# Optimization experiments

Measured on AMD Instinct MI355X. Metric: run time of the kernel, lower is better.

## Reference

```python
import jax, jax.numpy as jnp
import numpy as np

LN_EPS = 1e-5


def setup_inputs() -> dict:
    key = jax.random.key(0)
    k1, k2, k3, k4 = jax.random.split(key, 4)
    B, S, H, NH = 32, 256, 4096, 16
    scale = (2.0 ** 0.5) * ((3.0 / H) ** 0.5)
    inp = jax.random.normal(k1, (B, S, H), dtype=jnp.float32)
    mask = jax.random.randint(k2, (B, S), 0, 2, dtype=jnp.int32)  # 1 = padded key
    weight = jnp.ones((H,), dtype=jnp.float32)
    bias = jnp.zeros((H,), dtype=jnp.float32)
    qkv = jax.random.normal(k3, (H, 3 * H), dtype=jnp.float32) * scale
    o = jax.random.normal(k4, (H, H), dtype=jnp.float32) * scale
    return {"inp": inp, "mask": mask, "weight": weight, "bias": bias,
            "qkv": qkv, "o": o, "isPre": 1}


def _layer_norm(x, weight, bias):
    mu = jnp.mean(x, axis=-1, keepdims=True)
    var = jnp.mean(jnp.square(x - mu), axis=-1, keepdims=True)
    return (x - mu) * jax.lax.rsqrt(var + LN_EPS) * weight + bias


def _mha(x, mask, weight, bias, qkv, o, isPre, head_num=16):
    B, S, H = x.shape
    D = H // head_num
    xn = _layer_norm(x, weight, bias) if isPre else x
    # fused QKV projection: [B,S,3H]
    proj = jnp.einsum('bsh,hk->bsk', xn, qkv)
    q, k, v = jnp.split(proj, 3, axis=-1)
    q = q.reshape(B, S, head_num, D)
    k = k.reshape(B, S, head_num, D)
    v = v.reshape(B, S, head_num, D)
    scores = jnp.einsum('bqnd,bknd->bnqk', q, k) / jnp.sqrt(jnp.float32(D))
    # mask[b,k]==1 -> key k is padding, exclude from softmax
    neg = jnp.finfo(scores.dtype).min
    scores = jnp.where(mask[:, None, None, :] != 0, neg, scores)
    attn = jax.nn.softmax(scores, axis=-1)
    ctx = jnp.einsum('bnqk,bknd->bqnd', attn, v).reshape(B, S, H)
    out = jnp.einsum('bsh,ho->bso', ctx, o)
    if not isPre:
        out = _layer_norm(out, weight, bias)
    return out


def reference(inp, mask, weight, bias, qkv, o, isPre):
    return _mha(inp, mask, weight, bias, qkv, o, bool(isPre))
```

## Files before the change

kernel.cpp:

```cpp
#include <hip/hip_runtime.h>
#include <stdint.h>

typedef unsigned short u16;
typedef short bf16x8 __attribute__((ext_vector_type(8)));
typedef float f32x4 __attribute__((ext_vector_type(4)));
typedef unsigned short u16x8 __attribute__((ext_vector_type(8)));

#define MFMA16(a, b, c) __builtin_amdgcn_mfma_f32_16x16x32_bf16((a), (b), (c), 0, 0, 0)

#define GLOAD_LDS16(gp, lp)                                                        \
  __builtin_amdgcn_global_load_lds((const __attribute__((address_space(1))) void*)(gp), \
                                   (__attribute__((address_space(3))) void*)(lp), 16, 0, 0)

#define BARRIER asm volatile("s_barrier" ::: "memory")
#define WAITV(n) asm volatile("s_waitcnt vmcnt(" #n ")" ::: "memory")
#define WAITL0 asm volatile("s_waitcnt lgkmcnt(0)" ::: "memory")

__device__ __forceinline__ u16 f2bf(float x) {
  union { float f; uint32_t u; } v; v.f = x;
  uint32_t r = (v.u + 0x7FFFu + ((v.u >> 16) & 1u)) >> 16;
  return (u16)r;
}

__device__ __forceinline__ void do_transpose(const float* __restrict__ in,
                                             u16* __restrict__ out, int R, int C,
                                             int bid, float (*tile)[65], int t) {
  int nCt = C >> 6;
  int r0 = (bid / nCt) << 6, c0 = (bid % nCt) << 6;
  int r = t >> 2, cg = (t & 3) << 4;
  const float* src = in + (size_t)(r0 + r) * C + c0 + cg;
#pragma unroll
  for (int i = 0; i < 4; i++) {
    float4 v = *reinterpret_cast<const float4*>(src + (i << 2));
    tile[r][cg + (i << 2) + 0] = v.x; tile[r][cg + (i << 2) + 1] = v.y;
    tile[r][cg + (i << 2) + 2] = v.z; tile[r][cg + (i << 2) + 3] = v.w;
  }
  __syncthreads();
  int c = t >> 2, rg = (t & 3) << 4;
  u16* dst = out + (size_t)(c0 + c) * R + r0 + rg;
#pragma unroll
  for (int i = 0; i < 2; i++) {
    u16x8 o8;
#pragma unroll
    for (int j2 = 0; j2 < 8; j2++) o8[j2] = f2bf(tile[rg + (i << 3) + j2][c]);
    *reinterpret_cast<u16x8*>(dst + (i << 3)) = o8;
  }
}

__device__ __forceinline__ void do_ln(const float* __restrict__ in,
                                      const float* __restrict__ w,
                                      const float* __restrict__ bia,
                                      u16* __restrict__ out, int row,
                                      float* red, int t) {
  const float* x = in + (size_t)row * 4096;
  float4 v[4];
  float s = 0.f, sq = 0.f;
#pragma unroll
  for (int i = 0; i < 4; i++) {
    v[i] = *reinterpret_cast<const float4*>(x + i * 1024 + t * 4);
    s  += v[i].x + v[i].y + v[i].z + v[i].w;
    sq += v[i].x * v[i].x + v[i].y * v[i].y + v[i].z * v[i].z + v[i].w * v[i].w;
  }
#pragma unroll
  for (int off = 32; off > 0; off >>= 1) { s += __shfl_down(s, off); sq += __shfl_down(sq, off); }
  int wid = t >> 6, lane = t & 63;
  if (lane == 0) { red[wid] = s; red[4 + wid] = sq; }
  __syncthreads();
  if (t == 0) {
    float st = red[0] + red[1] + red[2] + red[3];
    float sqt = red[4] + red[5] + red[6] + red[7];
    float mu = st * (1.f / 4096.f);
    float var = sqt * (1.f / 4096.f) - mu * mu;
    red[0] = mu; red[1] = rsqrtf(var + 1e-5f);
  }
  __syncthreads();
  float mu = red[0], rs = red[1];
#pragma unroll
  for (int i = 0; i < 4; i++) {
    float4 wv = *reinterpret_cast<const float4*>(w + i * 1024 + t * 4);
    float4 bv = *reinterpret_cast<const float4*>(bia + i * 1024 + t * 4);
    ushort4 u;
    u.x = f2bf((v[i].x - mu) * rs * wv.x + bv.x);
    u.y = f2bf((v[i].y - mu) * rs * wv.y + bv.y);
    u.z = f2bf((v[i].z - mu) * rs * wv.z + bv.z);
    u.w = f2bf((v[i].w - mu) * rs * wv.w + bv.w);
    *reinterpret_cast<ushort4*>(out + (size_t)row * 4096 + i * 1024 + t * 4) = u;
  }
}

__global__ __launch_bounds__(256) void prep_fused(const float* __restrict__ qkvw, u16* __restrict__ qkvT,
                                                  const float* __restrict__ ow, u16* __restrict__ oT,
                                                  const float* __restrict__ inp, const float* __restrict__ w,
                                                  const float* __restrict__ bia, u16* __restrict__ xn) {
  __shared__ float tile[64][65];
  int bid = blockIdx.x, t = threadIdx.x;
  if (bid < 12288)      do_transpose(qkvw, qkvT, 4096, 12288, bid, tile, t);
  else if (bid < 16384) do_transpose(ow, oT, 4096, 4096, bid - 12288, tile, t);
  else                  do_ln(inp, w, bia, xn, bid - 16384, &tile[0][0], t);
}


#define LDA8(AR, Ab, mh) do {                                                     \
  _Pragma("unroll")                                                               \
  for (int mf = 0; mf < 4; mf++) {                                                \
    int lr = (mh)*128 + wm64 + mf*16 + llo;                                       \
    const char* rb = (Ab) + lr*128;                                               \
    int sw = (lr & 7) << 4;                                                       \
    AR[mf*2+0] = *reinterpret_cast<const bf16x8*>(rb + ((lhi16) ^ sw));           \
    AR[mf*2+1] = *reinterpret_cast<const bf16x8*>(rb + ((64 + lhi16) ^ sw));      \
  }                                                                               \
} while (0)

#define LDB4(BR, Bb, nh) do {                                                     \
  _Pragma("unroll")                                                               \
  for (int nf = 0; nf < 2; nf++) {                                                \
    int lr = (nh)*128 + wn32 + nf*16 + llo;                                       \
    const char* rb = (Bb) + lr*128;                                               \
    int sw = (lr & 7) << 4;                                                       \
    BR[nf*2+0] = *reinterpret_cast<const bf16x8*>(rb + ((lhi16) ^ sw));           \
    BR[nf*2+1] = *reinterpret_cast<const bf16x8*>(rb + ((64 + lhi16) ^ sw));      \
  }                                                                               \
} while (0)

#define MMAQ(AR, BR, mh, nh) do {                                                 \
  _Pragma("unroll")                                                               \
  for (int mf = 0; mf < 4; mf++)                                                  \
    _Pragma("unroll")                                                             \
    for (int nf = 0; nf < 2; nf++) {                                              \
      acc[(mh)*4+mf][(nh)*2+nf] = MFMA16(AR[mf*2+0], BR[nf*2+0], acc[(mh)*4+mf][(nh)*2+nf]); \
      acc[(mh)*4+mf][(nh)*2+nf] = MFMA16(AR[mf*2+1], BR[nf*2+1], acc[(mh)*4+mf][(nh)*2+nf]); \
    }                                                                             \
} while (0)

#define STAGE(isB, h, cbuf, ktile) do {                                           \
  const u16* g_ = (isB) ? Bt : A;                                                 \
  int base0_ = (isB) ? n0 : m0;                                                   \
  char* lb_ = smc + (cbuf)*65536 + (isB)*32768 + (h)*16384;                       \
  _Pragma("unroll")                                                               \
  for (int i_ = 0; i_ < 2; i_++) {                                                \
    int L_ = i_*512 + t;                                                          \
    int lr_ = (h)*128 + (L_ >> 3);                                                \
    int sl_ = (L_ & 7) ^ (lr_ & 7);                                               \
    int r_ = (isB) ? (((lr_ & 128) >> 2) | ((lr_ & 96) << 1) | (lr_ & 31))        \
                   : ((lr_ & 63) | ((lr_ & 64) << 1) | ((lr_ & 128) >> 1));       \
    GLOAD_LDS16(g_ + (size_t)(base0_ + r_) * K + (ktile)*64 + sl_*8, lb_ + L_*16);\
  }                                                                               \
} while (0)

#define TILE2(tt, S1, S2, W2) do {                                                \
  int c_ = (tt) & 1;                                                              \
  const char* Ab = smc + c_ * 65536;                                              \
  const char* Bb = Ab + 32768;                                                    \
          \
  LDA8(aR, Ab, 0); LDB4(b0R, Bb, 0); LDB4(b1R, Bb, 1);                            \
  if (S1) { STAGE(1, 0, c_ ^ 1, (tt) + 1); STAGE(0, 1, c_ ^ 1, (tt) + 1); }       \
  __builtin_amdgcn_s_setprio(1);                                                  \
  MMAQ(aR, b0R, 0, 0); MMAQ(aR, b1R, 0, 1);                                       \
  __builtin_amdgcn_s_setprio(0);                                                  \
  WAITL0; BARRIER;                                                                \
                                     \
  LDA8(aR, Ab, 1);                                                                \
  if (S2) { STAGE(0, 0, c_, (tt) + 2); STAGE(1, 1, c_, (tt) + 2); }               \
  __builtin_amdgcn_s_setprio(1);                                                  \
  MMAQ(aR, b1R, 1, 1); MMAQ(aR, b0R, 1, 0);                                       \
  __builtin_amdgcn_s_setprio(0);                                                  \
  WAITV(W2); WAITL0; BARRIER;                                                     \
} while (0)

template <int EPI>
__global__ __launch_bounds__(512, 2) void gemm256(const u16* __restrict__ A, const u16* __restrict__ Bt,
                                                  void* __restrict__ Cout, u16* __restrict__ vT,
                                                  int M, int N, int K, int nbn) {
  __shared__ u16 sm[65536];
  char* smc = (char*)sm;
  int bid = blockIdx.x;
  int s = bid >> 8, local = bid & 255;
  int xcd = local & 7, j = local >> 3;
  int trow = ((xcd >> 1) << 2) + (j >> 3);
  int tcol = ((xcd & 1) << 3) + (j & 7);
  int nsc = nbn >> 4;
  int sr = s / nsc, sc = s - sr * nsc;
  int tm = (sr << 4) + trow, tn = (sc << 4) + tcol;
  int m0 = tm << 8, n0 = tn << 8;
  int t = threadIdx.x;
  int w = t >> 6, lane = t & 63;
  int wm = w >> 2, wn = w & 3;
  int llo = lane & 15, lhi = lane >> 4;
  int wm64 = wm << 6, wn32 = wn << 5, lhi16 = lhi << 4;
  f32x4 acc[8][4] = {};
  bf16x8 aR[8], b0R[4], b1R[4];
  int NT = K >> 6;
  STAGE(0, 0, 0, 0); STAGE(1, 0, 0, 0); STAGE(1, 1, 0, 0); STAGE(0, 1, 0, 0);
  STAGE(0, 0, 1, 1); STAGE(1, 1, 1, 1);
  WAITV(4); BARRIER;
#pragma unroll 1
  for (int tt = 0; tt < NT - 2; ++tt) TILE2(tt, 1, 1, 4);
  TILE2(NT - 2, 1, 0, 0);
  TILE2(NT - 1, 0, 0, 0);
  if (EPI == 2) {
    float* C = (float*)Cout;
#pragma unroll
    for (int mi = 0; mi < 8; mi++)
#pragma unroll
      for (int ni = 0; ni < 4; ni++) {
        int m = m0 + wm * 128 + mi * 16 + lhi * 4;
        int n = n0 + wn * 64 + ni * 16 + llo;
#pragma unroll
        for (int r = 0; r < 4; r++) C[(size_t)(m + r) * N + n] = acc[mi][ni][r];
      }
  } else {
    if (n0 < 8192) {
      u16* qkb = (u16*)Cout;
#pragma unroll
      for (int mi = 0; mi < 8; mi++)
#pragma unroll
        for (int ni = 0; ni < 4; ni++) {
          int m = m0 + wm * 128 + mi * 16 + lhi * 4;
          int n = n0 + wn * 64 + ni * 16 + llo;
#pragma unroll
          for (int r = 0; r < 4; r++) qkb[(size_t)(m + r) * 8192 + n] = f2bf(acc[mi][ni][r]);
        }
    } else {
#pragma unroll
      for (int mi = 0; mi < 8; mi++)
#pragma unroll
        for (int ni = 0; ni < 4; ni++) {
          int m = m0 + wm * 128 + mi * 16 + lhi * 4;
          int n_ = n0 + wn * 64 + ni * 16 + llo - 8192;
          int h = n_ >> 8, d = n_ & 255;
          int b = m >> 8, s2 = m & 255;
          ushort4 u;
          u.x = f2bf(acc[mi][ni][0]); u.y = f2bf(acc[mi][ni][1]);
          u.z = f2bf(acc[mi][ni][2]); u.w = f2bf(acc[mi][ni][3]);
          *reinterpret_cast<ushort4*>(vT + ((size_t)((b << 4) + h) * 256 + d) * 256 + s2) = u;
        }
    }
  }
}

__global__ __launch_bounds__(512) void attn_kernel(const u16* __restrict__ qk,
                                                   const u16* __restrict__ vT,
                                                   const int* __restrict__ mask,
                                                   u16* __restrict__ ctx) {
  __shared__ u16 KV[2 * 32 * 1024 / 2];
  __shared__ u16 P[128 * 256];
  __shared__ float maskf[256];
  char* kv0 = (char*)KV;
  int bid = blockIdx.x;
  int half = bid & 1, h = (bid >> 1) & 15, b = bid >> 5;
  int bh = (b << 4) + h;
  int t = threadIdx.x, wid = t >> 6, lane = t & 63, llo = lane & 15, lhi = lane >> 4;
  if (t < 256) maskf[t] = mask[(b << 8) + t] ? -1e30f : 0.0f;
  bf16x8 qf[8];
  {
    const u16* qrow = qk + (size_t)((b << 8) + (half << 7) + (wid << 4) + llo) * 8192 + (h << 8);
#pragma unroll
    for (int c = 0; c < 8; c++)
      qf[c] = *reinterpret_cast<const bf16x8*>(qrow + (lhi << 3) + (c << 5));
  }
#define STAGE_K(kt, buf) do {                                                      \
    char* lb_ = kv0 + (buf) * 32768;                                               \
    _Pragma("unroll")                                                              \
    for (int i_ = 0; i_ < 4; i_++) {                                               \
      int G_ = (i_ << 9) + t;                                                      \
      int key_ = G_ >> 5, g_ = G_ & 31;                                            \
      int gs_ = g_ ^ (key_ & 7);                                                   \
      const u16* src_ = qk + (size_t)((b << 8) + ((kt) << 6) + key_) * 8192 + 4096 \
                        + (h << 8) + (gs_ << 3);                                   \
      GLOAD_LDS16(src_, lb_ + (G_ << 4));                                          \
    }                                                                              \
  } while (0)
#define STAGE_V(j, buf) do {                                                       \
    char* lb_ = kv0 + (buf) * 32768;                                               \
    _Pragma("unroll")                                                              \
    for (int i_ = 0; i_ < 4; i_++) {                                               \
      int G_ = (i_ << 9) + t;                                                      \
      int d_ = G_ >> 3, g_ = G_ & 7;                                               \
      int gs_ = g_ ^ (d_ & 7);                                                     \
      const u16* src_ = vT + ((size_t)bh * 256 + d_) * 256 + ((j) << 6) + (gs_ << 3); \
      GLOAD_LDS16(src_, lb_ + (G_ << 4));                                          \
    }                                                                              \
  } while (0)
  f32x4 sacc[16] = {};
  STAGE_K(0, 0);
#pragma unroll 1
  for (int kt = 0; kt < 4; kt++) {
    if (kt < 3) STAGE_K(kt + 1, (kt + 1) & 1); else STAGE_V(0, 0);
    WAITV(4); BARRIER;
    const char* kb0 = kv0 + (kt & 1) * 32768;
#pragma unroll
    for (int nf = 0; nf < 4; nf++) {
      int kl = (nf << 4) + llo;
      const char* kb = kb0 + (kl << 9);
      int sw = (kl & 7) << 4;
#pragma unroll
      for (int c = 0; c < 8; c++) {
        bf16x8 kf = *reinterpret_cast<const bf16x8*>(kb + (((lhi << 4) + (c << 6)) ^ sw));
        sacc[kt * 4 + nf] = MFMA16(qf[c], kf, sacc[kt * 4 + nf]);
      }
    }
    WAITL0; BARRIER;
  }
  float madd[16];
#pragma unroll
  for (int f = 0; f < 16; f++) madd[f] = maskf[(f << 4) + llo];
  float mx[4] = {-3e38f, -3e38f, -3e38f, -3e38f};
#pragma unroll
  for (int f = 0; f < 16; f++)
#pragma unroll
    for (int r = 0; r < 4; r++) {
      float sv = sacc[f][r] * 0.0625f + madd[f];
      sacc[f][r] = sv;
      mx[r] = fmaxf(mx[r], sv);
    }
#pragma unroll
  for (int r = 0; r < 4; r++)
#pragma unroll
    for (int d = 1; d < 16; d <<= 1) mx[r] = fmaxf(mx[r], __shfl_xor(mx[r], d));
  float sum[4] = {0.f, 0.f, 0.f, 0.f};
#pragma unroll
  for (int f = 0; f < 16; f++)
#pragma unroll
    for (int r = 0; r < 4; r++) {
      float p = __expf(sacc[f][r] - mx[r]);
      sacc[f][r] = p;
      sum[r] += p;
    }
#pragma unroll
  for (int r = 0; r < 4; r++)
#pragma unroll
    for (int d = 1; d < 16; d <<= 1) sum[r] += __shfl_xor(sum[r], d);
  float rin[4];
#pragma unroll
  for (int r = 0; r < 4; r++) rin[r] = 1.f / sum[r];
#pragma unroll
  for (int r = 0; r < 4; r++) {
    int q = (wid << 4) + (lhi << 2) + r;
    char* pb = (char*)P + (q << 9);
    int sw = (q & 7) << 4;
#pragma unroll
    for (int f = 0; f < 16; f++) {
      int key = (f << 4) + llo;
      *reinterpret_cast<u16*>(pb + ((key << 1) ^ sw)) = f2bf(sacc[f][r] * rin[r]);
    }
  }
  WAITL0;
  f32x4 cacc[16] = {};
#pragma unroll 1
  for (int j = 0; j < 4; j++) {
    if (j < 3) { STAGE_V(j + 1, (j + 1) & 1); WAITV(4); } else { WAITV(0); }
    BARRIER;
    const char* vb0 = kv0 + (j & 1) * 32768;
    bf16x8 pf[2];
    {
      int q = (wid << 4) + llo;
      const char* pb = (const char*)P + (q << 9);
      int sw = (q & 7) << 4;
#pragma unroll
      for (int c = 0; c < 2; c++)
        pf[c] = *reinterpret_cast<const bf16x8*>(pb + (((j << 7) + (c << 6) + (lhi << 4)) ^ sw));
    }
#pragma unroll
    for (int mf = 0; mf < 16; mf++) {
      int dl = (mf << 4) + llo;
      const char* vb = vb0 + (dl << 7);
      int sw = (dl & 7) << 4;
#pragma unroll
      for (int c = 0; c < 2; c++) {
        bf16x8 vf = *reinterpret_cast<const bf16x8*>(vb + (((lhi << 4) + (c << 6)) ^ sw));
        cacc[mf] = MFMA16(vf, pf[c], cacc[mf]);
      }
    }
    if (j < 3) { WAITL0; BARRIER; }
  }
#undef STAGE_K
#undef STAGE_V
  int token = (b << 8) + (half << 7) + (wid << 4) + llo;
  u16* crow = ctx + (size_t)token * 4096 + (h << 8);
#pragma unroll
  for (int mf = 0; mf < 16; mf++) {
    ushort4 u;
    u.x = f2bf(cacc[mf][0]); u.y = f2bf(cacc[mf][1]);
    u.z = f2bf(cacc[mf][2]); u.w = f2bf(cacc[mf][3]);
    *reinterpret_cast<ushort4*>(crow + (mf << 4) + (lhi << 2)) = u;
  }
}

extern "C" void kernel_launch(void* const* d_in, const int* in_sizes, int n_in,
                              void* d_out, int out_size, void* d_ws, size_t ws_size,
                              hipStream_t stream) {
  const float* inp  = (const float*)d_in[0];
  const int*   mask = (const int*)d_in[1];
  const float* w    = (const float*)d_in[2];
  const float* bia  = (const float*)d_in[3];
  const float* qkvw = (const float*)d_in[4];
  const float* ow   = (const float*)d_in[5];
  const size_t MB = 1024ull * 1024ull;
  if (ws_size < 352 * MB) return;
  char* ws = (char*)d_ws;
  u16* xn   = (u16*)(ws);
  u16* qkvT = (u16*)(ws + 64 * MB);
  u16* qk   = (u16*)(ws + 160 * MB);
  u16* vT   = (u16*)(ws + 288 * MB);
  u16* oT   = (u16*)(ws + 64 * MB + 48 * MB);
  (void)oT;
  if (ws_size < 384 * MB) return;
  u16* oT2  = (u16*)(ws + 352 * MB);
  u16* ctx  = (u16*)(ws);
  float* out = (float*)d_out;

  prep_fused<<<24576, 256, 0, stream>>>(qkvw, qkvT, ow, oT2, inp, w, bia, xn);
  gemm256<1><<<1536, 512, 0, stream>>>(xn, qkvT, (void*)qk, vT, 8192, 12288, 4096, 48);
  attn_kernel<<<1024, 512, 0, stream>>>(qk, vT, mask, ctx);
  gemm256<2><<<512, 512, 0, stream>>>(ctx, oT2, (void*)out, nullptr, 8192, 4096, 4096, 16);
}
```

Measured before the change: 1.230 ms.

## Load GEMM B operand directly from global into registers, halve LDS use

The B operand of the 256x256 bf16 GEMM no longer goes through LDS. Each wave now loads its B fragments straight from global memory into double-buffered registers, one k-tile ahead. Only A is staged through swizzled LDS, with a single-tile lookahead instead of two, which halves the shared memory footprint so two workgroups can fit per CU. The trade-off is that B rows are fetched redundantly by waves that share a column (relying on cache), global-load latency is exposed to the register path, and A prefetch depth is reduced.

```diff
diff --git a/kernel.cpp b/kernel.cpp
--- a/kernel.cpp
+++ b/kernel.cpp
@@ -111,14 +111,14 @@
   }                                                                               \
 } while (0)
 
-#define LDB4(BR, Bb, nh) do {                                                     \
+#define LDBD(BR0, BR1, ktile) do {                                                \
+  const u16* gb_ = Bt + (size_t)(n0 + wn64 + llo) * K + (ktile)*64 + (lhi << 3);  \
   _Pragma("unroll")                                                               \
   for (int nf = 0; nf < 2; nf++) {                                                \
-    int lr = (nh)*128 + wn32 + nf*16 + llo;                                       \
-    const char* rb = (Bb) + lr*128;                                               \
-    int sw = (lr & 7) << 4;                                                       \
-    BR[nf*2+0] = *reinterpret_cast<const bf16x8*>(rb + ((lhi16) ^ sw));           \
-    BR[nf*2+1] = *reinterpret_cast<const bf16x8*>(rb + ((64 + lhi16) ^ sw));      \
+    BR0[nf*2+0] = *reinterpret_cast<const bf16x8*>(gb_ + (size_t)(nf*16) * K);       \
+    BR0[nf*2+1] = *reinterpret_cast<const bf16x8*>(gb_ + (size_t)(nf*16) * K + 32);  \
+    BR1[nf*2+0] = *reinterpret_cast<const bf16x8*>(gb_ + (size_t)(32 + nf*16) * K);      \
+    BR1[nf*2+1] = *reinterpret_cast<const bf16x8*>(gb_ + (size_t)(32 + nf*16) * K + 32); \
   }                                                                               \
 } while (0)
 
@@ -132,46 +132,40 @@
     }                                                                             \
 } while (0)
 
-#define STAGE(isB, h, cbuf, ktile) do {                                           \
-  const u16* g_ = (isB) ? Bt : A;                                                 \
-  int base0_ = (isB) ? n0 : m0;                                                   \
-  char* lb_ = smc + (cbuf)*65536 + (isB)*32768 + (h)*16384;                       \
+#define STAGE_A(h, cbuf, ktile) do {                                              \
+  char* lb_ = smc + (cbuf)*32768 + (h)*16384;                                     \
   _Pragma("unroll")                                                               \
   for (int i_ = 0; i_ < 2; i_++) {                                                \
     int L_ = i_*512 + t;                                                          \
     int lr_ = (h)*128 + (L_ >> 3);                                                \
     int sl_ = (L_ & 7) ^ (lr_ & 7);                                               \
-    int r_ = (isB) ? (((lr_ & 128) >> 2) | ((lr_ & 96) << 1) | (lr_ & 31))        \
-                   : ((lr_ & 63) | ((lr_ & 64) << 1) | ((lr_ & 128) >> 1));       \
-    GLOAD_LDS16(g_ + (size_t)(base0_ + r_) * K + (ktile)*64 + sl_*8, lb_ + L_*16);\
+    int r_ = (lr_ & 63) | ((lr_ & 64) << 1) | ((lr_ & 128) >> 1);                 \
+    GLOAD_LDS16(A + (size_t)(m0 + r_) * K + (ktile)*64 + sl_*8, lb_ + L_*16);     \
   }                                                                               \
 } while (0)
 
-#define TILE2(tt, S1, S2, W2) do {                                                \
+#define TILE1(tt, S, BC0, BC1, BN0, BN1) do {                                     \
   int c_ = (tt) & 1;                                                              \
-  const char* Ab = smc + c_ * 65536;                                              \
-  const char* Bb = Ab + 32768;                                                    \
-          \
-  LDA8(aR, Ab, 0); LDB4(b0R, Bb, 0); LDB4(b1R, Bb, 1);                            \
-  if (S1) { STAGE(1, 0, c_ ^ 1, (tt) + 1); STAGE(0, 1, c_ ^ 1, (tt) + 1); }       \
+  const char* Ab = smc + c_ * 32768;                                              \
+  LDA8(aR, Ab, 0);                                                                \
+  if (S) { STAGE_A(0, c_ ^ 1, (tt) + 1); STAGE_A(1, c_ ^ 1, (tt) + 1); }          \
   __builtin_amdgcn_s_setprio(1);                                                  \
-  MMAQ(aR, b0R, 0, 0); MMAQ(aR, b1R, 0, 1);                                       \
+  MMAQ(aR, BC0, 0, 0); MMAQ(aR, BC1, 0, 1);                                       \
   __builtin_amdgcn_s_setprio(0);                                                  \
+  if (S) LDBD(BN0, BN1, (tt) + 1);                                                \
+  LDA8(aR, Ab, 1);                                                                \
+  __builtin_amdgcn_s_setprio(1);                                                  \
+  MMAQ(aR, BC1, 1, 1); MMAQ(aR, BC0, 1, 0);                                       \
+  __builtin_amdgcn_s_setprio(0);                                                  \
+  if (S) { WAITV(8); } else { WAITV(0); }                                         \
   WAITL0; BARRIER;                                                                \
-                                     \
-  LDA8(aR, Ab, 1);                                                                \
-  if (S2) { STAGE(0, 0, c_, (tt) + 2); STAGE(1, 1, c_, (tt) + 2); }               \
-  __builtin_amdgcn_s_setprio(1);                                                  \
-  MMAQ(aR, b1R, 1, 1); MMAQ(aR, b0R, 1, 0);                                       \
-  __builtin_amdgcn_s_setprio(0);                                                  \
-  WAITV(W2); WAITL0; BARRIER;                                                     \
 } while (0)
 
 template <int EPI>
 __global__ __launch_bounds__(512, 2) void gemm256(const u16* __restrict__ A, const u16* __restrict__ Bt,
                                                   void* __restrict__ Cout, u16* __restrict__ vT,
                                                   int M, int N, int K, int nbn) {
-  __shared__ u16 sm[65536];
+  __shared__ u16 sm[32768];
   char* smc = (char*)sm;
   int bid = blockIdx.x;
   int s = bid >> 8, local = bid & 255;
@@ -186,17 +180,20 @@
   int w = t >> 6, lane = t & 63;
   int wm = w >> 2, wn = w & 3;
   int llo = lane & 15, lhi = lane >> 4;
-  int wm64 = wm << 6, wn32 = wn << 5, lhi16 = lhi << 4;
+  int wm64 = wm << 6, wn64 = wn << 6, lhi16 = lhi << 4;
   f32x4 acc[8][4] = {};
-  bf16x8 aR[8], b0R[4], b1R[4];
+  bf16x8 aR[8], bA0[4], bA1[4], bB0[4], bB1[4];
   int NT = K >> 6;
-  STAGE(0, 0, 0, 0); STAGE(1, 0, 0, 0); STAGE(1, 1, 0, 0); STAGE(0, 1, 0, 0);
-  STAGE(0, 0, 1, 1); STAGE(1, 1, 1, 1);
-  WAITV(4); BARRIER;
+  STAGE_A(0, 0, 0); STAGE_A(1, 0, 0);
+  LDBD(bA0, bA1, 0);
+  WAITV(8); BARRIER;
 #pragma unroll 1
-  for (int tt = 0; tt < NT - 2; ++tt) TILE2(tt, 1, 1, 4);
-  TILE2(NT - 2, 1, 0, 0);
-  TILE2(NT - 1, 0, 0, 0);
+  for (int tt = 0; tt < NT - 2; tt += 2) {
+    TILE1(tt, 1, bA0, bA1, bB0, bB1);
+    TILE1(tt + 1, 1, bB0, bB1, bA0, bA1);
+  }
+  TILE1(NT - 2, 1, bA0, bA1, bB0, bB1);
+  TILE1(NT - 1, 0, bB0, bB1, bA0, bA1);
   if (EPI == 2) {
     float* C = (float*)Cout;
 #pragma unroll
@@ -396,15 +393,12 @@
   const float* qkvw = (const float*)d_in[4];
   const float* ow   = (const float*)d_in[5];
   const size_t MB = 1024ull * 1024ull;
-  if (ws_size < 352 * MB) return;
+  if (ws_size < 384 * MB) return;
   char* ws = (char*)d_ws;
   u16* xn   = (u16*)(ws);
   u16* qkvT = (u16*)(ws + 64 * MB);
   u16* qk   = (u16*)(ws + 160 * MB);
   u16* vT   = (u16*)(ws + 288 * MB);
-  u16* oT   = (u16*)(ws + 64 * MB + 48 * MB);
-  (void)oT;
-  if (ws_size < 384 * MB) return;
   u16* oT2  = (u16*)(ws + 352 * MB);
   u16* ctx  = (u16*)(ws);
   float* out = (float*)d_out;
```

Result: slower. 1.868 ms (+51.9%).
